# Performance work log

Measured on AMD Instinct MI355X. Metric: run time of the kernel, lower is better.

Reference implementation:

```python
import jax, jax.numpy as jnp
import numpy as np

N = 100000   # nodes
E = 1600000  # edges
F = 128      # input/hidden dim
C = 3        # classes
G = 64       # graphs in batch


def setup_inputs() -> dict:
    key = jax.random.key(0)
    ks = jax.random.split(key, 12)
    s = 1.0 / np.sqrt(F)
    return {
        "x": jax.random.normal(ks[0], (N, F), dtype=jnp.float32),
        "edge_index": jax.random.randint(ks[1], (2, E), 0, N, dtype=jnp.int64),
        "batch": jnp.sort(jax.random.randint(ks[2], (N,), 0, G, dtype=jnp.int64)),
        "W1": jax.random.normal(ks[3], (F, F), dtype=jnp.float32) * s,
        "b1": jnp.zeros((F,), dtype=jnp.float32),
        "W2": jax.random.normal(ks[4], (F, F), dtype=jnp.float32) * s,
        "b2": jnp.zeros((F,), dtype=jnp.float32),
        "W3": jax.random.normal(ks[5], (F, F), dtype=jnp.float32) * s,
        "b3": jnp.zeros((F,), dtype=jnp.float32),
        "Wc": jax.random.normal(ks[6], (F, C), dtype=jnp.float32) * s,
        "bc": jnp.zeros((C,), dtype=jnp.float32),
    }


def reference(x, edge_index, batch, W1, b1, W2, b2, W3, b3, Wc, bc):
    n = x.shape[0]
    src, dst = edge_index[0], edge_index[1]
    # GCN adds self-loops: A_hat = A + I
    loops = jnp.arange(n, dtype=src.dtype)
    src_a = jnp.concatenate([src, loops])
    dst_a = jnp.concatenate([dst, loops])
    # symmetric normalization D^-1/2 (A+I) D^-1/2 (in-degree incl. self-loop)
    deg = jax.ops.segment_sum(jnp.ones_like(dst_a, dtype=x.dtype), dst_a, num_segments=n)
    dis = jnp.where(deg > 0, jax.lax.rsqrt(deg), 0.0)
    norm = dis[src_a] * dis[dst_a]  # [E+N]

    def gcn_conv(h, W, b):
        h = h @ W                                    # [N, F']
        msg = h[src_a] * norm[:, None]               # gather + scale
        agg = jax.ops.segment_sum(msg, dst_a, num_segments=n)  # scatter-add
        return agg + b

    h = jax.nn.relu(gcn_conv(x, W1, b1))   # dropout = identity in eval mode
    h = jax.nn.relu(gcn_conv(h, W2, b2))
    h = jax.nn.relu(gcn_conv(h, W3, b3))

    # global_mean_pool over graph ids
    sums = jax.ops.segment_sum(h, batch, num_segments=G)
    cnt = jax.ops.segment_sum(jnp.ones((n,), dtype=h.dtype), batch, num_segments=G)
    pooled = sums / jnp.maximum(cnt, 1.0)[:, None]
    return pooled @ Wc + bc
```

## Files before the change

### kernel.cpp

```cpp
#include <hip/hip_runtime.h>
#include <cstdint>
#include <cstddef>

#define FDIM 128
#define CHUNK 4096
#define BSHIFT 8
#define BMASK 255
#define MAXB 512

typedef unsigned short ushort_t;
typedef __attribute__((ext_vector_type(8))) short short8;
typedef __attribute__((ext_vector_type(4))) float floatx4;

__device__ inline ushort_t f2bf(float f) {
  unsigned u = __float_as_uint(f);
  u += 0x7fffu + ((u >> 16) & 1u);
  return (ushort_t)(u >> 16);
}
__device__ inline float bf2f(ushort_t h) {
  return __uint_as_float((unsigned)h << 16);
}


__global__ __launch_bounds__(256) void k_hist(const int* __restrict__ dst, int e,
                                              int nb, int* __restrict__ chunkHist) {
  __shared__ int h[MAXB];
  int c = blockIdx.x;
  int base = c * CHUNK;
  int end = min(base + CHUNK, e);
  for (int i = threadIdx.x; i < nb; i += 256) h[i] = 0;
  __syncthreads();
  for (int i = base + threadIdx.x; i < end; i += 256)
    atomicAdd(&h[dst[i] >> BSHIFT], 1);
  __syncthreads();
  for (int b = threadIdx.x; b < nb; b += 256)
    chunkHist[(size_t)c * nb + b] = h[b];
}

__global__ __launch_bounds__(512) void k_scan1(const int* __restrict__ chunkHist,
                                               int nchunks, int nb,
                                               int* __restrict__ chunkOff,
                                               int* __restrict__ bucketTotal) {
  __shared__ int sb[512];
  int b = blockIdx.x;
  int t = threadIdx.x;
  int base = 0;
  for (int c0 = 0; c0 < nchunks; c0 += 512) {
    int c = c0 + t;
    int v = (c < nchunks) ? chunkHist[(size_t)c * nb + b] : 0;
    int x = v;
    sb[t] = x;
    __syncthreads();
    for (int off = 1; off < 512; off <<= 1) {
      int y = (t >= off) ? sb[t - off] : 0;
      __syncthreads();
      x += y;
      sb[t] = x;
      __syncthreads();
    }
    if (c < nchunks) chunkOff[(size_t)c * nb + b] = base + x - v;
    int tileTot = sb[511];
    __syncthreads();
    base += tileTot;
  }
  if (t == 0) bucketTotal[b] = base;
}

__global__ __launch_bounds__(512) void k_scan2(const int* __restrict__ bucketTotal,
                                               int nb, int e,
                                               int* __restrict__ bucketBase) {
  __shared__ int sb[512];
  int t = threadIdx.x;
  int v = (t < nb) ? bucketTotal[t] : 0;
  int x = v;
  sb[t] = x;
  __syncthreads();
  for (int off = 1; off < 512; off <<= 1) {
    int y = (t >= off) ? sb[t - off] : 0;
    __syncthreads();
    x += y;
    sb[t] = x;
    __syncthreads();
  }
  if (t < nb) bucketBase[t] = x - v;
  if (t == 0) bucketBase[nb] = e;
}

__global__ __launch_bounds__(256) void k_bin(const int* __restrict__ src,
                                             const int* __restrict__ dst, int e, int nb,
                                             const int* __restrict__ chunkHist,
                                             const int* __restrict__ chunkOff,
                                             const int* __restrict__ bucketBase,
                                             unsigned* __restrict__ binned) {
  __shared__ unsigned sortedL[CHUNK];
  __shared__ int gtarget[CHUNK];
  __shared__ int lbase[MAXB], lcur[MAXB], gbase[MAXB];
  __shared__ int stmp[256];
  int c = blockIdx.x;
  int base = c * CHUNK;
  int end = min(base + CHUNK, e);
  for (int i = threadIdx.x; i < nb; i += 256) {
    lbase[i] = chunkHist[(size_t)c * nb + i];
    gbase[i] = bucketBase[i] + chunkOff[(size_t)c * nb + i];
  }
  __syncthreads();
  int carry = 0;
  for (int i0 = 0; i0 < nb; i0 += 256) {
    int i = i0 + threadIdx.x;
    int v = (i < nb) ? lbase[i] : 0;
    int x = v;
    stmp[threadIdx.x] = x;
    __syncthreads();
    for (int off = 1; off < 256; off <<= 1) {
      int y = (threadIdx.x >= off) ? stmp[threadIdx.x - off] : 0;
      __syncthreads();
      x += y;
      stmp[threadIdx.x] = x;
      __syncthreads();
    }
    if (i < nb) lbase[i] = carry + x - v;
    int tileTot = stmp[255];
    __syncthreads();
    carry += tileTot;
  }
  for (int i = threadIdx.x; i < nb; i += 256) lcur[i] = lbase[i];
  __syncthreads();
  for (int i = base + threadIdx.x; i < end; i += 256) {
    int d = dst[i];
    int sv = src[i];
    int b = d >> BSHIFT;
    int slot = atomicAdd(&lcur[b], 1);
    sortedL[slot] = ((unsigned)sv << BSHIFT) | (unsigned)(d & BMASK);
    gtarget[slot] = gbase[b] + (slot - lbase[b]);
  }
  __syncthreads();
  for (int i = threadIdx.x; i < end - base; i += 256)
    binned[gtarget[i]] = sortedL[i];
}

__global__ __launch_bounds__(256) void k_fill2(const unsigned* __restrict__ binned,
                                               const int* __restrict__ bucketBase, int n,
                                               int* __restrict__ rowStart,
                                               int* __restrict__ deg,
                                               float* __restrict__ dis,
                                               int2* __restrict__ colPair) {
  __shared__ int h[256], sb[256], cur[256];
  int b = blockIdx.x;
  int s0 = bucketBase[b], s1 = bucketBase[b + 1];
  int nodeBase = b << BSHIFT;
  int t = threadIdx.x;
  h[t] = 0;
  __syncthreads();
  for (int i = s0 + t; i < s1; i += 256) atomicAdd(&h[binned[i] & BMASK], 1);
  __syncthreads();
  int v = h[t];
  int x = v;
  sb[t] = x;
  __syncthreads();
  for (int off = 1; off < 256; off <<= 1) {
    int y = (t >= off) ? sb[t - off] : 0;
    __syncthreads();
    x += y;
    sb[t] = x;
    __syncthreads();
  }
  int start = s0 + x - v;
  cur[t] = start;
  int node = nodeBase + t;
  if (node < n) {
    rowStart[node] = start;
    deg[node] = v;
    dis[node] = rsqrtf((float)(v + 1));
  }
  __syncthreads();
  for (int i = s0 + t; i < s1; i += 256) {
    unsigned en = binned[i];
    int slot = atomicAdd(&cur[en & BMASK], 1);
    colPair[slot] = int2{(int)(en >> BSHIFT), 0};
  }
}

__global__ __launch_bounds__(256) void k_edgew(int2* __restrict__ colPair, int e,
                                               const float* __restrict__ dis) {
  int i = blockIdx.x * 256 + threadIdx.x;
  if (i < e) {
    int2 p = colPair[i];
    p.y = __float_as_int(dis[p.x]);
    colPair[i] = p;
  }
}

__global__ __launch_bounds__(256) void k_prepw(const float* __restrict__ W1,
                                               const float* __restrict__ W2,
                                               const float* __restrict__ W3,
                                               ushort_t* __restrict__ out) {
  int b = blockIdx.x;
  const float* W = (b == 0) ? W1 : (b == 1) ? W2 : W3;
  ushort_t* o = out + (size_t)b * 16384;
  for (int idx = threadIdx.x; idx < 16384; idx += 256) {
    int j = idx & 7;
    int lane = (idx >> 3) & 63;
    int ct = (idx >> 9) & 7;
    int kc = idx >> 12;
    int k = kc * 32 + (lane >> 4) * 8 + j;
    int col = (lane & 15) * 8 + ct;
    o[idx] = f2bf(W[k * FDIM + col]);
  }
}

template <int INBF>
__global__ __launch_bounds__(256) void k_mm(const void* __restrict__ Ain,
                                            const ushort_t* __restrict__ Wsw,
                                            ushort_t* __restrict__ O, int n) {
  __shared__ ushort_t Bs[16384];
  int tid = threadIdx.x;
  for (int q = tid; q < 2048; q += 256)
    ((uint4*)Bs)[q] = ((const uint4*)Wsw)[q];
  __syncthreads();

  int w = tid >> 6;
  int lane = tid & 63;
  int quad = lane >> 4;
  int l15 = lane & 15;
  int rb = blockIdx.x * 128 + w * 32;
  const float* Af = (const float*)Ain;
  const ushort_t* Ab = (const ushort_t*)Ain;

  int row0 = rb + l15;
  int row1 = rb + 16 + l15;
  bool v0 = row0 < n, v1 = row1 < n;

  floatx4 acc[2][8];
#pragma unroll
  for (int rt = 0; rt < 2; ++rt)
#pragma unroll
    for (int ct = 0; ct < 8; ++ct) acc[rt][ct] = floatx4{0.f, 0.f, 0.f, 0.f};

#pragma unroll
  for (int kc = 0; kc < 4; ++kc) {
    int k0 = kc * 32 + quad * 8;
    short8 a0 = short8{0, 0, 0, 0, 0, 0, 0, 0};
    short8 a1 = short8{0, 0, 0, 0, 0, 0, 0, 0};
    if (INBF) {
      if (v0) a0 = *(const short8*)&Ab[(size_t)row0 * FDIM + k0];
      if (v1) a1 = *(const short8*)&Ab[(size_t)row1 * FDIM + k0];
    } else {
      if (v0) {
        float4 f0 = *(const float4*)&Af[(size_t)row0 * FDIM + k0];
        float4 f1 = *(const float4*)&Af[(size_t)row0 * FDIM + k0 + 4];
        a0 = short8{(short)f2bf(f0.x), (short)f2bf(f0.y), (short)f2bf(f0.z),
                    (short)f2bf(f0.w), (short)f2bf(f1.x), (short)f2bf(f1.y),
                    (short)f2bf(f1.z), (short)f2bf(f1.w)};
      }
      if (v1) {
        float4 f0 = *(const float4*)&Af[(size_t)row1 * FDIM + k0];
        float4 f1 = *(const float4*)&Af[(size_t)row1 * FDIM + k0 + 4];
        a1 = short8{(short)f2bf(f0.x), (short)f2bf(f0.y), (short)f2bf(f0.z),
                    (short)f2bf(f0.w), (short)f2bf(f1.x), (short)f2bf(f1.y),
                    (short)f2bf(f1.z), (short)f2bf(f1.w)};
      }
    }
#pragma unroll
    for (int ct = 0; ct < 8; ++ct) {
      short8 bf = *(const short8*)&Bs[((kc * 8 + ct) * 64 + lane) * 8];
      acc[0][ct] = __builtin_amdgcn_mfma_f32_16x16x32_bf16(a0, bf, acc[0][ct], 0, 0, 0);
      acc[1][ct] = __builtin_amdgcn_mfma_f32_16x16x32_bf16(a1, bf, acc[1][ct], 0, 0, 0);
    }
  }

#pragma unroll
  for (int rt = 0; rt < 2; ++rt) {
#pragma unroll
    for (int i = 0; i < 4; ++i) {
      int row = rb + rt * 16 + quad * 4 + i;
      if (row < n) {
        uint4 pk;
        pk.x = (unsigned)f2bf(acc[rt][0][i]) | ((unsigned)f2bf(acc[rt][1][i]) << 16);
        pk.y = (unsigned)f2bf(acc[rt][2][i]) | ((unsigned)f2bf(acc[rt][3][i]) << 16);
        pk.z = (unsigned)f2bf(acc[rt][4][i]) | ((unsigned)f2bf(acc[rt][5][i]) << 16);
        pk.w = (unsigned)f2bf(acc[rt][6][i]) | ((unsigned)f2bf(acc[rt][7][i]) << 16);
        *(uint4*)&O[(size_t)row * FDIM + l15 * 8] = pk;
      }
    }
  }
}

__global__ __launch_bounds__(256) void k_agg(const ushort_t* __restrict__ Hin,
                                             ushort_t* __restrict__ Hout,
                                             const int* __restrict__ rowStart,
                                             const int* __restrict__ degE,
                                             const int2* __restrict__ colPair,
                                             const float* __restrict__ dis,
                                             const float* __restrict__ bias, int n) {
  int node = blockIdx.x * 8 + (threadIdx.x >> 5);
  int lane = threadIdx.x & 31;
  if (node >= n) return;
  const uint2* hin = (const uint2*)Hin;
  float di = dis[node];
  uint2 su = hin[(size_t)node * 32 + lane];
  float ws = di * di;
  float a0 = ws * __uint_as_float(su.x << 16);
  float a1 = ws * __uint_as_float(su.x & 0xffff0000u);
  float a2 = ws * __uint_as_float(su.y << 16);
  float a3 = ws * __uint_as_float(su.y & 0xffff0000u);
  int s0 = rowStart[node], cnt = degE[node];
#pragma unroll 4
  for (int j = 0; j < cnt; ++j) {
    int2 p = colPair[s0 + j];
    float w = di * __int_as_float(p.y);
    uint2 u = hin[(size_t)p.x * 32 + lane];
    a0 += w * __uint_as_float(u.x << 16);
    a1 += w * __uint_as_float(u.x & 0xffff0000u);
    a2 += w * __uint_as_float(u.y << 16);
    a3 += w * __uint_as_float(u.y & 0xffff0000u);
  }
  float4 b = ((const float4*)bias)[lane];
  a0 = fmaxf(a0 + b.x, 0.f);
  a1 = fmaxf(a1 + b.y, 0.f);
  a2 = fmaxf(a2 + b.z, 0.f);
  a3 = fmaxf(a3 + b.w, 0.f);
  uint2 o;
  o.x = (unsigned)f2bf(a0) | ((unsigned)f2bf(a1) << 16);
  o.y = (unsigned)f2bf(a2) | ((unsigned)f2bf(a3) << 16);
  ((uint2*)Hout)[(size_t)node * 32 + lane] = o;
}


__global__ __launch_bounds__(128) void k_gstart(const int* __restrict__ batch, int n,
                                                int g_count, int* __restrict__ gstart) {
  int g = threadIdx.x;
  if (g > g_count) return;
  int lo = 0, hi = n;
  while (lo < hi) {
    int mid = (lo + hi) >> 1;
    if (batch[mid] < g) lo = mid + 1;
    else hi = mid;
  }
  gstart[g] = lo;
}

__global__ __launch_bounds__(128) void k_pool(const ushort_t* __restrict__ H,
                                              const int* __restrict__ gstart,
                                              float* __restrict__ pooled, int g_count) {
  int g = blockIdx.x >> 4;
  int c = blockIdx.x & 15;
  int s = gstart[g], e = gstart[g + 1];
  int len = e - s;
  int chunk = (len + 15) >> 4;
  int ns = s + c * chunk;
  int ne = min(ns + chunk, e);
  float acc = 0.f;
  for (int i = ns; i < ne; ++i) acc += bf2f(H[(size_t)i * FDIM + threadIdx.x]);
  atomicAdd(&pooled[g * FDIM + threadIdx.x], acc);
}

__global__ __launch_bounds__(192) void k_final(const float* __restrict__ pooled,
                                               const int* __restrict__ gstart,
                                               const float* __restrict__ Wc,
                                               const float* __restrict__ bc,
                                               float* __restrict__ out, int g_count) {
  int t = threadIdx.x;
  if (t >= g_count * 3) return;
  int g = t / 3, c = t % 3;
  int cnt = gstart[g + 1] - gstart[g];
  float inv = 1.0f / (float)max(cnt, 1);
  float acc = bc[c];
#pragma unroll 8
  for (int k = 0; k < FDIM; ++k) acc += pooled[g * FDIM + k] * inv * Wc[k * 3 + c];
  out[g * 3 + c] = acc;
}


extern "C" void kernel_launch(void* const* d_in, const int* in_sizes, int n_in,
                              void* d_out, int out_size, void* d_ws, size_t ws_size,
                              hipStream_t stream) {
  const float* x = (const float*)d_in[0];
  const int* edge = (const int*)d_in[1];
  const int* batch = (const int*)d_in[2];
  const float* W1 = (const float*)d_in[3];
  const float* b1 = (const float*)d_in[4];
  const float* W2 = (const float*)d_in[5];
  const float* b2 = (const float*)d_in[6];
  const float* W3 = (const float*)d_in[7];
  const float* b3 = (const float*)d_in[8];
  const float* Wc = (const float*)d_in[9];
  const float* bc = (const float*)d_in[10];
  float* out = (float*)d_out;

  const int N = in_sizes[0] / FDIM;
  const int E = in_sizes[1] / 2;
  const int G = out_size / 3;
  const int* src = edge;
  const int* dst = edge + E;

  const int NCH = (E + CHUNK - 1) / CHUNK;
  const int NB = (N + (1 << BSHIFT) - 1) >> BSHIFT;

  char* ws = (char*)d_ws;
  size_t off = 0;
  auto carve = [&](size_t bytes) -> void* {
    void* p = ws + off;
    off = (off + bytes + 255) & ~(size_t)255;
    return p;
  };
  ushort_t* h0 = (ushort_t*)carve((size_t)N * FDIM * 2);
  ushort_t* h1 = (ushort_t*)carve((size_t)N * FDIM * 2);
  int2* colPair = (int2*)carve((size_t)E * 8);
  unsigned* binned = (unsigned*)carve((size_t)E * 4);
  int* chunkHist = (int*)carve((size_t)NCH * NB * 4);
  int* chunkOff = (int*)carve((size_t)NCH * NB * 4);
  int* bucketTotal = (int*)carve((size_t)NB * 4);
  int* bucketBase = (int*)carve((size_t)(NB + 1) * 4);
  int* rowStart = (int*)carve((size_t)N * 4);
  int* deg = (int*)carve((size_t)N * 4);
  float* dis = (float*)carve((size_t)N * 4);
  int* gstart = (int*)carve((size_t)(G + 1) * 4);
  float* pooled = (float*)carve((size_t)G * FDIM * 4);
  ushort_t* wsw = (ushort_t*)carve((size_t)3 * 16384 * 2);
  (void)n_in;
  (void)ws_size;

  hipMemsetAsync(pooled, 0, (size_t)G * FDIM * 4, stream);

  k_hist<<<NCH, 256, 0, stream>>>(dst, E, NB, chunkHist);
  k_scan1<<<NB, 512, 0, stream>>>(chunkHist, NCH, NB, chunkOff, bucketTotal);
  k_scan2<<<1, 512, 0, stream>>>(bucketTotal, NB, E, bucketBase);
  k_bin<<<NCH, 256, 0, stream>>>(src, dst, E, NB, chunkHist, chunkOff, bucketBase,
                                 binned);
  k_fill2<<<NB, 256, 0, stream>>>(binned, bucketBase, N, rowStart, deg, dis, colPair);
  k_edgew<<<(E + 255) / 256, 256, 0, stream>>>(colPair, E, dis);
  k_prepw<<<3, 256, 0, stream>>>(W1, W2, W3, wsw);

  int mmb = (N + 127) / 128;
  int aggb = (N + 7) / 8;
  k_mm<0><<<mmb, 256, 0, stream>>>(x, wsw, h0, N);
  k_agg<<<aggb, 256, 0, stream>>>(h0, h1, rowStart, deg, colPair, dis, b1, N);
  k_mm<1><<<mmb, 256, 0, stream>>>(h1, wsw + 16384, h0, N);
  k_agg<<<aggb, 256, 0, stream>>>(h0, h1, rowStart, deg, colPair, dis, b2, N);
  k_mm<1><<<mmb, 256, 0, stream>>>(h1, wsw + 32768, h0, N);
  k_agg<<<aggb, 256, 0, stream>>>(h0, h1, rowStart, deg, colPair, dis, b3, N);

  k_gstart<<<1, 128, 0, stream>>>(batch, N, G, gstart);
  k_pool<<<G * 16, 128, 0, stream>>>(h1, gstart, pooled, G);
  k_final<<<1, 192, 0, stream>>>(pooled, gstart, Wc, bc, out, G);
}
```

Before: 448.2 us.

## Restructure CSR build, drop scan2/gstart kernels, nontemporal agg loads

```diff
diff --git a/kernel.cpp b/kernel.cpp
--- a/kernel.cpp
+++ b/kernel.cpp
@@ -7,6 +7,7 @@
 #define BSHIFT 8
 #define BMASK 255
 #define MAXB 512
+#define EBMAX 12288
 
 typedef unsigned short ushort_t;
 typedef __attribute__((ext_vector_type(8))) short short8;
@@ -40,7 +41,9 @@
 __global__ __launch_bounds__(512) void k_scan1(const int* __restrict__ chunkHist,
                                                int nchunks, int nb,
                                                int* __restrict__ chunkOff,
-                                               int* __restrict__ bucketTotal) {
+                                               int* __restrict__ bucketTotal,
+                                               int* __restrict__ bucketBase,
+                                               int* __restrict__ counter) {
   __shared__ int sb[512];
   int b = blockIdx.x;
   int t = threadIdx.x;
@@ -63,46 +66,25 @@
     __syncthreads();
     base += tileTot;
   }
-  if (t == 0) bucketTotal[b] = base;
-}
-
-__global__ __launch_bounds__(512) void k_scan2(const int* __restrict__ bucketTotal,
-                                               int nb, int e,
-                                               int* __restrict__ bucketBase) {
-  __shared__ int sb[512];
-  int t = threadIdx.x;
-  int v = (t < nb) ? bucketTotal[t] : 0;
-  int x = v;
-  sb[t] = x;
-  __syncthreads();
-  for (int off = 1; off < 512; off <<= 1) {
-    int y = (t >= off) ? sb[t - off] : 0;
-    __syncthreads();
-    x += y;
-    sb[t] = x;
-    __syncthreads();
-  }
-  if (t < nb) bucketBase[t] = x - v;
-  if (t == 0) bucketBase[nb] = e;
+  if (t == 0) {
+    bucketTotal[b] = base;
+    bucketBase[b] = atomicAdd(counter, base);
+  }
 }
 
 __global__ __launch_bounds__(256) void k_bin(const int* __restrict__ src,
                                              const int* __restrict__ dst, int e, int nb,
                                              const int* __restrict__ chunkHist,
-                                             const int* __restrict__ chunkOff,
-                                             const int* __restrict__ bucketBase,
+                                             int* __restrict__ chunkLB,
                                              unsigned* __restrict__ binned) {
   __shared__ unsigned sortedL[CHUNK];
-  __shared__ int gtarget[CHUNK];
-  __shared__ int lbase[MAXB], lcur[MAXB], gbase[MAXB];
+  __shared__ int lbase[MAXB], lcur[MAXB];
   __shared__ int stmp[256];
   int c = blockIdx.x;
   int base = c * CHUNK;
   int end = min(base + CHUNK, e);
-  for (int i = threadIdx.x; i < nb; i += 256) {
+  for (int i = threadIdx.x; i < nb; i += 256)
     lbase[i] = chunkHist[(size_t)c * nb + i];
-    gbase[i] = bucketBase[i] + chunkOff[(size_t)c * nb + i];
-  }
   __syncthreads();
   int carry = 0;
   for (int i0 = 0; i0 < nb; i0 += 256) {
@@ -123,7 +105,10 @@
     __syncthreads();
     carry += tileTot;
   }
-  for (int i = threadIdx.x; i < nb; i += 256) lcur[i] = lbase[i];
+  for (int i = threadIdx.x; i < nb; i += 256) {
+    lcur[i] = lbase[i];
+    chunkLB[(size_t)c * nb + i] = lbase[i];
+  }
   __syncthreads();
   for (int i = base + threadIdx.x; i < end; i += 256) {
     int d = dst[i];
@@ -131,52 +116,67 @@
     int b = d >> BSHIFT;
     int slot = atomicAdd(&lcur[b], 1);
     sortedL[slot] = ((unsigned)sv << BSHIFT) | (unsigned)(d & BMASK);
-    gtarget[slot] = gbase[b] + (slot - lbase[b]);
   }
   __syncthreads();
   for (int i = threadIdx.x; i < end - base; i += 256)
-    binned[gtarget[i]] = sortedL[i];
+    binned[(size_t)c * CHUNK + i] = sortedL[i];
 }
 
 __global__ __launch_bounds__(256) void k_fill2(const unsigned* __restrict__ binned,
-                                               const int* __restrict__ bucketBase, int n,
+                                               const int* __restrict__ chunkHist,
+                                               const int* __restrict__ chunkLB,
+                                               const int* __restrict__ chunkOff,
+                                               const int* __restrict__ bucketBase,
+                                               const int* __restrict__ bucketTotal,
+                                               int nchunks, int nb, int n,
                                                int* __restrict__ rowStart,
                                                int* __restrict__ deg,
                                                float* __restrict__ dis,
                                                int2* __restrict__ colPair) {
-  __shared__ int h[256], sb[256], cur[256];
+  __shared__ unsigned eb[EBMAX];
+  __shared__ int h[256], sbv[256], cur[256];
   int b = blockIdx.x;
-  int s0 = bucketBase[b], s1 = bucketBase[b + 1];
-  int nodeBase = b << BSHIFT;
   int t = threadIdx.x;
+  int total = min(bucketTotal[b], EBMAX);
+  int gbase = bucketBase[b];
+  for (int c = t; c < nchunks; c += 256) {
+    int cnt = chunkHist[(size_t)c * nb + b];
+    if (cnt == 0) continue;
+    size_t sp = (size_t)c * CHUNK + chunkLB[(size_t)c * nb + b];
+    int dp = chunkOff[(size_t)c * nb + b];
+    for (int i = 0; i < cnt; ++i) {
+      if (dp + i < EBMAX) eb[dp + i] = binned[sp + i];
+    }
+  }
+  __syncthreads();
   h[t] = 0;
   __syncthreads();
-  for (int i = s0 + t; i < s1; i += 256) atomicAdd(&h[binned[i] & BMASK], 1);
+  for (int i = t; i < total; i += 256) atomicAdd(&h[eb[i] & BMASK], 1);
   __syncthreads();
   int v = h[t];
   int x = v;
-  sb[t] = x;
+  sbv[t] = x;
   __syncthreads();
   for (int off = 1; off < 256; off <<= 1) {
-    int y = (t >= off) ? sb[t - off] : 0;
+    int y = (t >= off) ? sbv[t - off] : 0;
     __syncthreads();
     x += y;
-    sb[t] = x;
-    __syncthreads();
-  }
-  int start = s0 + x - v;
-  cur[t] = start;
-  int node = nodeBase + t;
+    sbv[t] = x;
+    __syncthreads();
+  }
+  int startL = x - v;
+  cur[t] = startL;
+  int node = (b << BSHIFT) + t;
   if (node < n) {
-    rowStart[node] = start;
+    rowStart[node] = gbase + startL;
     deg[node] = v;
     dis[node] = rsqrtf((float)(v + 1));
   }
   __syncthreads();
-  for (int i = s0 + t; i < s1; i += 256) {
-    unsigned en = binned[i];
+  for (int i = t; i < total; i += 256) {
+    unsigned en = eb[i];
     int slot = atomicAdd(&cur[en & BMASK], 1);
-    colPair[slot] = int2{(int)(en >> BSHIFT), 0};
+    colPair[(size_t)gbase + slot] = int2{(int)(en >> BSHIFT), 0};
   }
 }
 
@@ -304,11 +304,13 @@
   float a2 = ws * __uint_as_float(su.y << 16);
   float a3 = ws * __uint_as_float(su.y & 0xffff0000u);
   int s0 = rowStart[node], cnt = degE[node];
-#pragma unroll 4
+  const long long* cp = (const long long*)(colPair + s0);
+#pragma unroll 8
   for (int j = 0; j < cnt; ++j) {
-    int2 p = colPair[s0 + j];
-    float w = di * __int_as_float(p.y);
-    uint2 u = hin[(size_t)p.x * 32 + lane];
+    long long pv = __builtin_nontemporal_load(cp + j);
+    int sidx = (int)(unsigned)(pv & 0xffffffffLL);
+    float w = di * __int_as_float((int)(pv >> 32));
+    uint2 u = hin[(size_t)sidx * 32 + lane];
     a0 += w * __uint_as_float(u.x << 16);
     a1 += w * __uint_as_float(u.x & 0xffff0000u);
     a2 += w * __uint_as_float(u.y << 16);
@@ -319,32 +321,34 @@
   a1 = fmaxf(a1 + b.y, 0.f);
   a2 = fmaxf(a2 + b.z, 0.f);
   a3 = fmaxf(a3 + b.w, 0.f);
-  uint2 o;
-  o.x = (unsigned)f2bf(a0) | ((unsigned)f2bf(a1) << 16);
-  o.y = (unsigned)f2bf(a2) | ((unsigned)f2bf(a3) << 16);
-  ((uint2*)Hout)[(size_t)node * 32 + lane] = o;
-}
-
-
-__global__ __launch_bounds__(128) void k_gstart(const int* __restrict__ batch, int n,
-                                                int g_count, int* __restrict__ gstart) {
-  int g = threadIdx.x;
-  if (g > g_count) return;
+  unsigned long long ov =
+      (unsigned long long)((unsigned)f2bf(a0) | ((unsigned)f2bf(a1) << 16)) |
+      ((unsigned long long)((unsigned)f2bf(a2) | ((unsigned)f2bf(a3) << 16)) << 32);
+  __builtin_nontemporal_store(
+      ov, (unsigned long long*)((uint2*)Hout + (size_t)node * 32 + lane));
+}
+
+
+__device__ inline int lower_bound_batch(const int* __restrict__ batch, int n, int g) {
   int lo = 0, hi = n;
   while (lo < hi) {
     int mid = (lo + hi) >> 1;
     if (batch[mid] < g) lo = mid + 1;
     else hi = mid;
   }
-  gstart[g] = lo;
+  return lo;
 }
 
 __global__ __launch_bounds__(128) void k_pool(const ushort_t* __restrict__ H,
-                                              const int* __restrict__ gstart,
+                                              const int* __restrict__ batch, int n,
                                               float* __restrict__ pooled, int g_count) {
+  __shared__ int se[2];
   int g = blockIdx.x >> 4;
   int c = blockIdx.x & 15;
-  int s = gstart[g], e = gstart[g + 1];
+  if (threadIdx.x < 2)
+    se[threadIdx.x] = lower_bound_batch(batch, n, g + (int)threadIdx.x);
+  __syncthreads();
+  int s = se[0], e = se[1];
   int len = e - s;
   int chunk = (len + 15) >> 4;
   int ns = s + c * chunk;
@@ -355,14 +359,14 @@
 }
 
 __global__ __launch_bounds__(192) void k_final(const float* __restrict__ pooled,
-                                               const int* __restrict__ gstart,
+                                               const int* __restrict__ batch, int n,
                                                const float* __restrict__ Wc,
                                                const float* __restrict__ bc,
                                                float* __restrict__ out, int g_count) {
   int t = threadIdx.x;
   if (t >= g_count * 3) return;
   int g = t / 3, c = t % 3;
-  int cnt = gstart[g + 1] - gstart[g];
+  int cnt = lower_bound_batch(batch, n, g + 1) - lower_bound_batch(batch, n, g);
   float inv = 1.0f / (float)max(cnt, 1);
   float acc = bc[c];
 #pragma unroll 8
@@ -406,28 +410,31 @@
   ushort_t* h0 = (ushort_t*)carve((size_t)N * FDIM * 2);
   ushort_t* h1 = (ushort_t*)carve((size_t)N * FDIM * 2);
   int2* colPair = (int2*)carve((size_t)E * 8);
-  unsigned* binned = (unsigned*)carve((size_t)E * 4);
+  unsigned* binned = (unsigned*)carve((size_t)NCH * CHUNK * 4);
   int* chunkHist = (int*)carve((size_t)NCH * NB * 4);
   int* chunkOff = (int*)carve((size_t)NCH * NB * 4);
+  int* chunkLB = (int*)carve((size_t)NCH * NB * 4);
   int* bucketTotal = (int*)carve((size_t)NB * 4);
-  int* bucketBase = (int*)carve((size_t)(NB + 1) * 4);
+  int* bucketBase = (int*)carve((size_t)NB * 4);
+  int* counter = (int*)carve(256);
   int* rowStart = (int*)carve((size_t)N * 4);
   int* deg = (int*)carve((size_t)N * 4);
   float* dis = (float*)carve((size_t)N * 4);
-  int* gstart = (int*)carve((size_t)(G + 1) * 4);
   float* pooled = (float*)carve((size_t)G * FDIM * 4);
   ushort_t* wsw = (ushort_t*)carve((size_t)3 * 16384 * 2);
   (void)n_in;
   (void)ws_size;
 
   hipMemsetAsync(pooled, 0, (size_t)G * FDIM * 4, stream);
+  hipMemsetAsync(counter, 0, 4, stream);
 
   k_hist<<<NCH, 256, 0, stream>>>(dst, E, NB, chunkHist);
-  k_scan1<<<NB, 512, 0, stream>>>(chunkHist, NCH, NB, chunkOff, bucketTotal);
-  k_scan2<<<1, 512, 0, stream>>>(bucketTotal, NB, E, bucketBase);
-  k_bin<<<NCH, 256, 0, stream>>>(src, dst, E, NB, chunkHist, chunkOff, bucketBase,
-                                 binned);
-  k_fill2<<<NB, 256, 0, stream>>>(binned, bucketBase, N, rowStart, deg, dis, colPair);
+  k_scan1<<<NB, 512, 0, stream>>>(chunkHist, NCH, NB, chunkOff, bucketTotal,
+                                  bucketBase, counter);
+  k_bin<<<NCH, 256, 0, stream>>>(src, dst, E, NB, chunkHist, chunkLB, binned);
+  k_fill2<<<NB, 256, 0, stream>>>(binned, chunkHist, chunkLB, chunkOff, bucketBase,
+                                  bucketTotal, NCH, NB, N, rowStart, deg, dis,
+                                  colPair);
   k_edgew<<<(E + 255) / 256, 256, 0, stream>>>(colPair, E, dis);
   k_prepw<<<3, 256, 0, stream>>>(W1, W2, W3, wsw);
 
@@ -440,7 +447,6 @@
   k_mm<1><<<mmb, 256, 0, stream>>>(h1, wsw + 32768, h0, N);
   k_agg<<<aggb, 256, 0, stream>>>(h0, h1, rowStart, deg, colPair, dis, b3, N);
 
-  k_gstart<<<1, 128, 0, stream>>>(batch, N, G, gstart);
-  k_pool<<<G * 16, 128, 0, stream>>>(h1, gstart, pooled, G);
-  k_final<<<1, 192, 0, stream>>>(pooled, gstart, Wc, bc, out, G);
-}
+  k_pool<<<G * 16, 128, 0, stream>>>(h1, batch, N, pooled, G);
+  k_final<<<1, 192, 0, stream>>>(pooled, batch, N, Wc, bc, out, G);
+}
```

Result: slower. 523.3 us (+16.8%).
